# Performance work log

Hardware: AMD Instinct MI355X
Metric: run time of the kernel (lower is better)

The kernel has to match this reference:

```python
import jax, jax.numpy as jnp
import numpy as np

B, S, D, H = 2, 2048, 1024, 16
DH = D // H  # dim_per_head = 64


def setup_inputs() -> dict:
    key = jax.random.key(0)
    ks = jax.random.split(key, 12)
    scale = 1.0 / np.sqrt(D)
    inp = {
        "key": jax.random.normal(ks[0], (B, S, D), jnp.float32),
        "value": jax.random.normal(ks[1], (B, S, D), jnp.float32),
        "query": jax.random.normal(ks[2], (B, S, D), jnp.float32),
        "mask": jnp.zeros((B, S, S), dtype=bool),
        # nn.Linear weights stored as [out, in]; we keep [in, out] for x @ W
        "Wk": jax.random.normal(ks[3], (D, D), jnp.float32) * scale,
        "bk": jnp.zeros((D,), jnp.float32),
        "Wv": jax.random.normal(ks[4], (D, D), jnp.float32) * scale,
        "bv": jnp.zeros((D,), jnp.float32),
        "Wq": jax.random.normal(ks[5], (D, D), jnp.float32) * scale,
        "bq": jnp.zeros((D,), jnp.float32),
        "Wo": jax.random.normal(ks[6], (D, D), jnp.float32) * scale,
        "bo": jnp.zeros((D,), jnp.float32),
    }
    return inp


def reference(key, value, query, mask, Wk, bk, Wv, bv, Wq, bq, Wo, bo):
    # project and split heads: [B, S, D] -> [B, H, S, DH]
    def shape(x):
        return x.reshape(B, S, H, DH).transpose(0, 2, 1, 3)

    k = shape(key @ Wk + bk)
    v = shape(value @ Wv + bv)
    q = shape(query @ Wq + bq) / jnp.sqrt(jnp.asarray(DH, key.dtype))

    # scores: [B, H, Sq, Sk]
    scores = jnp.einsum("bhqd,bhkd->bhqk", q, k)
    scores = jnp.where(mask[:, None, :, :], jnp.asarray(-1e10, scores.dtype), scores)
    attn = jax.nn.softmax(scores, axis=-1)
    # dropout is identity in eval mode
    context = jnp.einsum("bhqk,bhkd->bhqd", attn, v)
    context = context.transpose(0, 2, 1, 3).reshape(B, S, D)
    output = context @ Wo + bo
    return output, attn
```

## Files before the change

kernel.cpp:

```cpp
#include <hip/hip_runtime.h>

#define B_  2
#define S_  2048
#define D_  1024
#define H_  16

typedef _Float16 h8 __attribute__((ext_vector_type(8)));
typedef _Float16 h4 __attribute__((ext_vector_type(4)));
typedef float f4 __attribute__((ext_vector_type(4)));

static __device__ __forceinline__ f4 mfma16(h8 a, h8 b, f4 c) {
  return __builtin_amdgcn_mfma_f32_16x16x32_f16(a, b, c, 0, 0, 0);
}

static __device__ __forceinline__ void gload16(const void* g, void* l) {
  __builtin_amdgcn_global_load_lds(
      (const __attribute__((address_space(1))) void*)g,
      (__attribute__((address_space(3))) void*)l, 16, 0, 0);
}

struct C3 { const float* in[3]; _Float16* out[3]; };
__global__ __launch_bounds__(256) void cvt3_kernel(C3 c) {
  const float* in = c.in[blockIdx.y];
  _Float16* out = c.out[blockIdx.y];
  const size_t i = ((size_t)blockIdx.x * 256 + threadIdx.x) * 8;
  float4 a = *(const float4*)(in + i);
  float4 b = *(const float4*)(in + i + 4);
  h8 v;
  v[0]=(_Float16)a.x; v[1]=(_Float16)a.y; v[2]=(_Float16)a.z; v[3]=(_Float16)a.w;
  v[4]=(_Float16)b.x; v[5]=(_Float16)b.y; v[6]=(_Float16)b.z; v[7]=(_Float16)b.w;
  *(h8*)(out + i) = v;
}

struct W4 { const float* w[4]; _Float16* wt[4]; };
__global__ __launch_bounds__(256) void wtrans4_kernel(W4 a) {
  const float* W = a.w[blockIdx.z];
  _Float16* WT = a.wt[blockIdx.z];
  __shared__ float tile[64][65];
  const int t = threadIdx.x;
  const int bi = blockIdx.x * 64;
  const int bj = blockIdx.y * 64;
  const int row = t >> 2, c0 = (t & 3) * 16;
  const float* src = W + (size_t)(bi + row) * D_ + bj + c0;
#pragma unroll
  for (int j = 0; j < 4; j++) {
    float4 v = *(const float4*)(src + j * 4);
    tile[row][c0 + j*4 + 0] = v.x; tile[row][c0 + j*4 + 1] = v.y;
    tile[row][c0 + j*4 + 2] = v.z; tile[row][c0 + j*4 + 3] = v.w;
  }
  __syncthreads();
  h8 o0, o1;
#pragma unroll
  for (int j = 0; j < 8; j++) o0[j] = (_Float16)tile[c0 + j][row];
#pragma unroll
  for (int j = 0; j < 8; j++) o1[j] = (_Float16)tile[c0 + 8 + j][row];
  _Float16* dst = WT + (size_t)(bj + row) * D_ + bi + c0;
  *(h8*)(dst)     = o0;
  *(h8*)(dst + 8) = o1;
}

__global__ __launch_bounds__(256) void maskflag_kernel(const unsigned char* __restrict__ mask,
                                                       unsigned char* __restrict__ flags) {
  __shared__ int s;
  const int t = threadIdx.x;
  const int kt = blockIdx.x, qb = blockIdx.y, b = blockIdx.z;
  if (t == 0) s = 0;
  __syncthreads();
  const unsigned char* mp = mask + ((size_t)(b * S_ + qb * 128 + (t >> 1))) * S_
                          + kt * 64 + (t & 1) * 32;
  const uint4* p = (const uint4*)mp;
  uint4 v = p[0], w = p[1];
  unsigned int o = v.x | v.y | v.z | v.w | w.x | w.y | w.z | w.w;
  if (o) s = 1;
  __syncthreads();
  if (t == 0) flags[((size_t)b * 16 + qb) * 32 + kt] = (unsigned char)s;
}

struct GArg { const _Float16* A; const _Float16* BT; const float* bias;
              void* out; float scale; int mode; };
struct G3 { GArg a[3]; };

__global__ __launch_bounds__(256, 3) void gemmp_kernel(G3 G) {
  const GArg g = G.a[blockIdx.z];
  const _Float16* __restrict__ A  = g.A;
  const _Float16* __restrict__ BT = g.BT;
  __shared__ _Float16 Ash[128 * 64];
  __shared__ _Float16 Bsh[128 * 64];
  const int t = threadIdx.x, lane = t & 63, wave = t >> 6;
  const int lrow = lane & 15, lq = lane >> 4;
  const int m0 = blockIdx.x * 128, n0 = blockIdx.y * 128;
  const int wm = wave >> 1, wn = wave & 1;
  f4 acc[4][4];
#pragma unroll
  for (int i = 0; i < 4; i++)
#pragma unroll
    for (int j = 0; j < 4; j++) acc[i][j] = f4{0.f, 0.f, 0.f, 0.f};
  float bb[4];
#pragma unroll
  for (int j = 0; j < 4; j++) bb[j] = g.bias[n0 + wn*64 + j*16 + lrow];

  const int srow = t >> 3;
  const int lch  = (t & 7) ^ (srow & 7);
  const _Float16* asrc = A  + (size_t)(m0 + srow) * D_ + lch * 8;
  const _Float16* bsrc = BT + (size_t)(n0 + srow) * D_ + lch * 8;

  for (int k0 = 0; k0 < D_; k0 += 64) {
#pragma unroll
    for (int rnd = 0; rnd < 4; rnd++)
      gload16(asrc + (size_t)(rnd * 32) * D_ + k0,
              (char*)Ash + rnd * 4096 + wave * 1024);
#pragma unroll
    for (int rnd = 0; rnd < 4; rnd++)
      gload16(bsrc + (size_t)(rnd * 32) * D_ + k0,
              (char*)Bsh + rnd * 4096 + wave * 1024);
    __syncthreads();
#pragma unroll
    for (int kf = 0; kf < 2; kf++) {
      h8 af[4], bf[4];
#pragma unroll
      for (int i = 0; i < 4; i++) {
        int rr = wm*64 + i*16 + lrow;
        int ch = (kf*4 + lq) ^ (rr & 7);
        af[i] = *(h8*)((char*)Ash + rr*128 + ch*16);
      }
#pragma unroll
      for (int j = 0; j < 4; j++) {
        int rr = wn*64 + j*16 + lrow;
        int ch = (kf*4 + lq) ^ (rr & 7);
        bf[j] = *(h8*)((char*)Bsh + rr*128 + ch*16);
      }
#pragma unroll
      for (int i = 0; i < 4; i++)
#pragma unroll
        for (int j = 0; j < 4; j++)
          acc[i][j] = mfma16(af[i], bf[j], acc[i][j]);
    }
    __syncthreads();
  }

  if (g.mode == 0) {
    _Float16* out = (_Float16*)g.out;
#pragma unroll
    for (int i = 0; i < 4; i++) {
      int m = m0 + wm*64 + i*16 + lq*4;
#pragma unroll
      for (int j = 0; j < 4; j++) {
        int n = n0 + wn*64 + j*16 + lrow;
#pragma unroll
        for (int r = 0; r < 4; r++)
          out[(size_t)(m + r) * D_ + n] = (_Float16)((acc[i][j][r] + bb[j]) * g.scale);
      }
    }
  } else if (g.mode == 1) {
    _Float16* out = (_Float16*)g.out;
#pragma unroll
    for (int i = 0; i < 4; i++) {
      int m = m0 + wm*64 + i*16 + lq*4;
      int b = m >> 11, s = m & (S_ - 1);
#pragma unroll
      for (int j = 0; j < 4; j++) {
        int n = n0 + wn*64 + j*16 + lrow;
        int hh = n >> 6, dh = n & 63;
        h4 hv;
#pragma unroll
        for (int r = 0; r < 4; r++) hv[r] = (_Float16)(acc[i][j][r] + bb[j]);
        *(h4*)(out + ((size_t)((b * H_ + hh) * 64 + dh)) * S_ + s) = hv;
      }
    }
  } else {
    float* out = (float*)g.out;
#pragma unroll
    for (int i = 0; i < 4; i++) {
      int m = m0 + wm*64 + i*16 + lq*4;
#pragma unroll
      for (int j = 0; j < 4; j++) {
        int n = n0 + wn*64 + j*16 + lrow;
#pragma unroll
        for (int r = 0; r < 4; r++)
          out[(size_t)(m + r) * D_ + n] = acc[i][j][r] + bb[j];
      }
    }
  }
}

__global__ __launch_bounds__(512, 4) void gemmz_kernel(G3 G) {
  const GArg g = G.a[blockIdx.z];
  const _Float16* __restrict__ A  = g.A;
  const _Float16* __restrict__ BT = g.BT;
  __shared__ _Float16 Ash[128 * 64];
  __shared__ _Float16 Bsh[128 * 64];
  const int t = threadIdx.x, lane = t & 63, wave = t >> 6;
  const int lrow = lane & 15, lq = lane >> 4;
  const int m0 = blockIdx.x * 128, n0 = blockIdx.y * 128;
  const int wm = wave >> 2, wn = wave & 3;
  f4 acc[4][2];
#pragma unroll
  for (int i = 0; i < 4; i++)
#pragma unroll
    for (int j = 0; j < 2; j++) acc[i][j] = f4{0.f, 0.f, 0.f, 0.f};
  float bb[2];
#pragma unroll
  for (int j = 0; j < 2; j++) bb[j] = g.bias[n0 + wn*32 + j*16 + lrow];

  const int srow = t >> 3;
  const int lch  = (t & 7) ^ (srow & 7);
  const _Float16* a0 = A  + (size_t)(m0 + srow)      * D_ + lch * 8;
  const _Float16* a1 = A  + (size_t)(m0 + 64 + srow) * D_ + lch * 8;
  const _Float16* b0 = BT + (size_t)(n0 + srow)      * D_ + lch * 8;
  const _Float16* b1 = BT + (size_t)(n0 + 64 + srow) * D_ + lch * 8;
  char* adst0 = (char*)Ash + wave * 1024;
  char* adst1 = (char*)Ash + 8192 + wave * 1024;
  char* bdst0 = (char*)Bsh + wave * 1024;
  char* bdst1 = (char*)Bsh + 8192 + wave * 1024;

  for (int k0 = 0; k0 < D_; k0 += 64) {
    gload16(a0 + k0, adst0);
    gload16(a1 + k0, adst1);
    gload16(b0 + k0, bdst0);
    gload16(b1 + k0, bdst1);
    __syncthreads();
#pragma unroll
    for (int kf = 0; kf < 2; kf++) {
      h8 af[4], bf[2];
#pragma unroll
      for (int i = 0; i < 4; i++) {
        int rr = wm*64 + i*16 + lrow;
        int ch = (kf*4 + lq) ^ (rr & 7);
        af[i] = *(h8*)((char*)Ash + rr*128 + ch*16);
      }
#pragma unroll
      for (int j = 0; j < 2; j++) {
        int rr = wn*32 + j*16 + lrow;
        int ch = (kf*4 + lq) ^ (rr & 7);
        bf[j] = *(h8*)((char*)Bsh + rr*128 + ch*16);
      }
#pragma unroll
      for (int i = 0; i < 4; i++)
#pragma unroll
        for (int j = 0; j < 2; j++)
          acc[i][j] = mfma16(af[i], bf[j], acc[i][j]);
    }
    __syncthreads();
  }

  if (g.mode == 0) {
    _Float16* out = (_Float16*)g.out;
#pragma unroll
    for (int i = 0; i < 4; i++) {
      int m = m0 + wm*64 + i*16 + lq*4;
#pragma unroll
      for (int j = 0; j < 2; j++) {
        int n = n0 + wn*32 + j*16 + lrow;
#pragma unroll
        for (int r = 0; r < 4; r++)
          out[(size_t)(m + r) * D_ + n] = (_Float16)((acc[i][j][r] + bb[j]) * g.scale);
      }
    }
  } else if (g.mode == 1) {
    _Float16* out = (_Float16*)g.out;
#pragma unroll
    for (int i = 0; i < 4; i++) {
      int m = m0 + wm*64 + i*16 + lq*4;
      int b = m >> 11, s = m & (S_ - 1);
#pragma unroll
      for (int j = 0; j < 2; j++) {
        int n = n0 + wn*32 + j*16 + lrow;
        int hh = n >> 6, dh = n & 63;
        h4 hv;
#pragma unroll
        for (int r = 0; r < 4; r++) hv[r] = (_Float16)(acc[i][j][r] + bb[j]);
        *(h4*)(out + ((size_t)((b * H_ + hh) * 64 + dh)) * S_ + s) = hv;
      }
    }
  } else {
    float* out = (float*)g.out;
#pragma unroll
    for (int i = 0; i < 4; i++) {
      int m = m0 + wm*64 + i*16 + lq*4;
#pragma unroll
      for (int j = 0; j < 2; j++) {
        int n = n0 + wn*32 + j*16 + lrow;
#pragma unroll
        for (int r = 0; r < 4; r++)
          out[(size_t)(m + r) * D_ + n] = acc[i][j][r] + bb[j];
      }
    }
  }
}


__global__ __launch_bounds__(256, 4) void attnA_kernel(
    const _Float16* __restrict__ Qp, const _Float16* __restrict__ Kp,
    const unsigned char* __restrict__ mask, const unsigned char* __restrict__ flags,
    float* __restrict__ Lbuf)
{
  __shared__ _Float16 Kt[256 * 64];
  const int t = threadIdx.x, lane = t & 63, wave = t >> 6;
  const int lrow = lane & 15, lq = lane >> 4;
  const int logical = ((blockIdx.x & 7) << 7) + (blockIdx.x >> 3);
  const int bh = logical >> 5, qb = logical & 31;
  const int b = bh >> 4, h = bh & 15;
  const int q0 = qb * 64, qw = q0 + wave * 16;

  h8 qf0, qf1;
  {
    const _Float16* qp = Qp + ((size_t)(b * S_ + qw + lrow)) * D_ + h * 64 + lq * 8;
    qf0 = *(const h8*)qp;
    qf1 = *(const h8*)(qp + 32);
  }

  const int srow = t >> 3, klch = (t & 7) ^ (srow & 7);
  const _Float16* ksrc = Kp + ((size_t)(b * S_ + srow)) * D_ + h * 64 + klch * 8;
  char* kdst = (char*)Kt + wave * 1024;
  const unsigned char* mflags = flags + ((size_t)(b * 16 + (qb >> 1))) * 32;

  float lsum[4] = {0.f, 0.f, 0.f, 0.f};
  for (int kt = 0; kt < S_; kt += 256) {
#pragma unroll
    for (int rnd = 0; rnd < 8; rnd++)
      gload16(ksrc + (size_t)(kt + rnd * 32) * D_, kdst + rnd * 4096);
    __syncthreads();
    const unsigned char* mrow = mask + ((size_t)(b * S_ + qw + lq*4)) * S_ + kt + lrow;
#pragma unroll
    for (int c = 0; c < 16; c++) {
      int kr = c*16 + lrow, sx = kr & 7;
      h8 k0 = *(h8*)((char*)Kt + kr*128 + ((lq     ^ sx) << 4));
      h8 k1 = *(h8*)((char*)Kt + kr*128 + (((4+lq) ^ sx) << 4));
      f4 a = f4{0.f, 0.f, 0.f, 0.f};
      a = mfma16(qf0, k0, a);
      a = mfma16(qf1, k1, a);
      if (mflags[(kt >> 6) + (c >> 2)]) {
#pragma unroll
        for (int r = 0; r < 4; r++)
          if (mrow[(size_t)r * S_ + c*16]) a[r] = -1e10f;
      }
#pragma unroll
      for (int r = 0; r < 4; r++) lsum[r] += __expf(fminf(a[r], 75.f));
    }
    __syncthreads();
  }

#pragma unroll
  for (int r = 0; r < 4; r++) {
    float cs = lsum[r];
#pragma unroll
    for (int d = 1; d < 16; d <<= 1) cs += __shfl_xor(cs, d);
    if (lrow == 0) Lbuf[((size_t)bh << 11) + qw + lq*4 + r] = 1.0f / cs;
  }
}

__global__ __launch_bounds__(256, 4) void attnB_kernel(
    const _Float16* __restrict__ Qp, const _Float16* __restrict__ Kp,
    const _Float16* __restrict__ VpT, const unsigned char* __restrict__ mask,
    const unsigned char* __restrict__ flags, const float* __restrict__ Lbuf,
    float* __restrict__ attn, _Float16* __restrict__ CtxH)
{
  __shared__ _Float16 Kt[128 * 64];
  __shared__ _Float16 Vt[64 * 128];
  __shared__ _Float16 Pt[64 * 64];
  const int t = threadIdx.x, lane = t & 63, wave = t >> 6;
  const int lrow = lane & 15, lq = lane >> 4;
  const int logical = ((blockIdx.x & 7) << 7) + (blockIdx.x >> 3);
  const int bh = logical >> 5, qb = logical & 31;
  const int b = bh >> 4, h = bh & 15;
  const int q0 = qb * 64, qw = q0 + wave * 16;

  h8 qf0, qf1;
  {
    const _Float16* qp = Qp + ((size_t)(b * S_ + qw + lrow)) * D_ + h * 64 + lq * 8;
    qf0 = *(const h8*)qp;
    qf1 = *(const h8*)(qp + 32);
  }
  float li[4];
#pragma unroll
  for (int r = 0; r < 4; r++) li[r] = Lbuf[((size_t)bh << 11) + qw + lq*4 + r];

  const int srow = t >> 3, klch = (t & 7) ^ (srow & 7);
  const _Float16* ksrc = Kp + ((size_t)(b * S_ + srow)) * D_ + h * 64 + klch * 8;
  char* kdst = (char*)Kt + wave * 1024;
  const int vrow = t >> 4, vlch = (t & 15) ^ (vrow & 15);
  const _Float16* vsrc = VpT + (size_t)bh * 64 * S_ + (size_t)vrow * S_ + vlch * 8;
  char* vdst = (char*)Vt + wave * 1024;
  const unsigned char* mflags = flags + ((size_t)(b * 16 + (qb >> 1))) * 32;

  f4 ctx[4];
#pragma unroll
  for (int dt = 0; dt < 4; dt++) ctx[dt] = f4{0.f, 0.f, 0.f, 0.f};

  for (int kt = 0; kt < S_; kt += 128) {
#pragma unroll
    for (int rnd = 0; rnd < 4; rnd++)
      gload16(ksrc + (size_t)(kt + rnd * 32) * D_, kdst + rnd * 4096);
#pragma unroll
    for (int rnd = 0; rnd < 4; rnd++)
      gload16(vsrc + (size_t)(rnd * 16) * S_ + kt, vdst + rnd * 4096);
    __syncthreads();

#pragma unroll
    for (int hh = 0; hh < 2; hh++) {
      const int kbase = kt + hh * 64;
      const bool mf = mflags[kbase >> 6] != 0;
      const unsigned char* mrow = mask + ((size_t)(b * S_ + qw + lq*4)) * S_ + kbase + lrow;
      const int prw = wave*16 + lq*4;
#pragma unroll
      for (int c = 0; c < 4; c++) {
        int kr = hh*64 + c*16 + lrow, sx = kr & 7;
        h8 k0 = *(h8*)((char*)Kt + kr*128 + ((lq     ^ sx) << 4));
        h8 k1 = *(h8*)((char*)Kt + kr*128 + (((4+lq) ^ sx) << 4));
        f4 a = f4{0.f, 0.f, 0.f, 0.f};
        a = mfma16(qf0, k0, a);
        a = mfma16(qf1, k1, a);
        if (mf) {
#pragma unroll
          for (int r = 0; r < 4; r++)
            if (mrow[(size_t)r * S_ + c*16]) a[r] = -1e10f;
        }
        float* ap = attn + ((size_t)bh * S_ + qw + lq*4) * S_ + kbase + c*16 + lrow;
        int eb = c*32 + lrow*2;
#pragma unroll
        for (int r = 0; r < 4; r++) {
          float p = __expf(fminf(a[r], 75.f)) * li[r];
          ap[(size_t)r * S_] = p;
          int rw = prw + r;
          *(_Float16*)((char*)Pt + rw*128 + ((((eb >> 4) ^ (rw & 7))) << 4) + (eb & 15))
              = (_Float16)p;
        }
      }
      {
        int pr2 = wave*16 + lrow, sxp = pr2 & 7;
        h8 pf0 = *(h8*)((char*)Pt + pr2*128 + (((    lq) ^ sxp) << 4));
        h8 pf1 = *(h8*)((char*)Pt + pr2*128 + (((4 + lq) ^ sxp) << 4));
#pragma unroll
        for (int dt = 0; dt < 4; dt++) {
          int vr = dt*16 + lrow, sxv = vr & 15;
          h8 vf0 = *(h8*)((char*)Vt + vr*256 + (((hh*8     + lq) ^ sxv) << 4));
          h8 vf1 = *(h8*)((char*)Vt + vr*256 + (((hh*8 + 4 + lq) ^ sxv) << 4));
          ctx[dt] = mfma16(pf0, vf0, ctx[dt]);
          ctx[dt] = mfma16(pf1, vf1, ctx[dt]);
        }
      }
    }
    __syncthreads();
  }

  _Float16* cp = CtxH + ((size_t)(b * S_ + qw + lq*4)) * D_ + h * 64 + lrow;
#pragma unroll
  for (int dt = 0; dt < 4; dt++)
#pragma unroll
    for (int r = 0; r < 4; r++)
      cp[(size_t)r * D_ + dt*16] = (_Float16)ctx[dt][r];
}

extern "C" void kernel_launch(void* const* d_in, const int* in_sizes, int n_in,
                              void* d_out, int out_size, void* d_ws, size_t ws_size,
                              hipStream_t stream) {
  const float* key   = (const float*)d_in[0];
  const float* value = (const float*)d_in[1];
  const float* query = (const float*)d_in[2];
  const unsigned char* mask = (const unsigned char*)d_in[3];
  const float* Wk = (const float*)d_in[4];
  const float* bk = (const float*)d_in[5];
  const float* Wv = (const float*)d_in[6];
  const float* bv = (const float*)d_in[7];
  const float* Wq = (const float*)d_in[8];
  const float* bq = (const float*)d_in[9];
  const float* Wo = (const float*)d_in[10];
  const float* bo = (const float*)d_in[11];

  char* ws = (char*)d_ws;
  _Float16* WkT  = (_Float16*)(ws + 0);
  _Float16* WvT  = (_Float16*)(ws + (size_t)2  * 1024 * 1024);
  _Float16* WqT  = (_Float16*)(ws + (size_t)4  * 1024 * 1024);
  _Float16* WoT  = (_Float16*)(ws + (size_t)6  * 1024 * 1024);
  _Float16* Qp   = (_Float16*)(ws + (size_t)8  * 1024 * 1024);
  _Float16* Kp   = (_Float16*)(ws + (size_t)16 * 1024 * 1024);
  _Float16* VpT  = (_Float16*)(ws + (size_t)24 * 1024 * 1024);
  _Float16* CtxH = (_Float16*)(ws + (size_t)32 * 1024 * 1024);
  unsigned char* flags = (unsigned char*)(ws + (size_t)40 * 1024 * 1024);
  float* Lbuf = (float*)(ws + (size_t)40 * 1024 * 1024 + 64 * 1024);

  float* outp = (float*)d_out;
  float* attn = outp + (size_t)B_ * S_ * D_;
  _Float16* qH = (_Float16*)(attn);
  _Float16* kH = (_Float16*)((char*)attn + (size_t)8  * 1024 * 1024);
  _Float16* vH = (_Float16*)((char*)attn + (size_t)16 * 1024 * 1024);

  C3 c{{query, key, value}, {qH, kH, vH}};
  cvt3_kernel<<<dim3(2048, 3), 256, 0, stream>>>(c);

  W4 w{{Wk, Wv, Wq, Wo}, {WkT, WvT, WqT, WoT}};
  wtrans4_kernel<<<dim3(16, 16, 4), 256, 0, stream>>>(w);

  maskflag_kernel<<<dim3(32, 16, 2), 256, 0, stream>>>(mask, flags);

  G3 gp{{{qH, WqT, bq, Qp, 0.125f, 0},
         {kH, WkT, bk, Kp, 1.0f,   0},
         {vH, WvT, bv, VpT, 1.0f,  1}}};
  gemmp_kernel<<<dim3(32, 8, 3), 256, 0, stream>>>(gp);

  attnA_kernel<<<1024, 256, 0, stream>>>(Qp, Kp, mask, flags, Lbuf);
  attnB_kernel<<<1024, 256, 0, stream>>>(Qp, Kp, VpT, mask, flags, Lbuf, attn, CtxH);

  G3 go{{{CtxH, WoT, bo, outp, 1.0f, 2},
         {nullptr, nullptr, nullptr, nullptr, 0.f, 2},
         {nullptr, nullptr, nullptr, nullptr, 0.f, 2}}};
  gemmz_kernel<<<dim3(32, 8, 1), 512, 0, stream>>>(go);
}
```

Measured before the change: 298.0 us.

## Fuse attention row-sum and output passes into one kernel with MFMA priority

Merges the two attention kernels into one. Each block first computes the softmax denominators over all keys, then reuses them in registers for the second pass that writes the attention probabilities and context, with one shared-memory buffer holding both phases. This drops a kernel launch and the round trip of the normalizer buffer through global memory, and reloads Q only once. It also raises wave priority around the MFMA sections so matrix work is issued ahead of other waves. Shared memory grows to 40KB per block, which may limit how many blocks fit on each CU.

```diff
diff --git a/kernel.cpp b/kernel.cpp
--- a/kernel.cpp
+++ b/kernel.cpp
@@ -288,13 +288,13 @@
   }
 }
 
-
-__global__ __launch_bounds__(256, 4) void attnA_kernel(
+__global__ __launch_bounds__(256, 4) void attnF_kernel(
     const _Float16* __restrict__ Qp, const _Float16* __restrict__ Kp,
-    const unsigned char* __restrict__ mask, const unsigned char* __restrict__ flags,
-    float* __restrict__ Lbuf)
+    const _Float16* __restrict__ VpT, const unsigned char* __restrict__ mask,
+    const unsigned char* __restrict__ flags,
+    float* __restrict__ attn, _Float16* __restrict__ CtxH)
 {
-  __shared__ _Float16 Kt[256 * 64];
+  __shared__ char smem[40960];
   const int t = threadIdx.x, lane = t & 63, wave = t >> 6;
   const int lrow = lane & 15, lq = lane >> 4;
   const int logical = ((blockIdx.x & 7) << 7) + (blockIdx.x >> 3);
@@ -311,8 +311,9 @@
 
   const int srow = t >> 3, klch = (t & 7) ^ (srow & 7);
   const _Float16* ksrc = Kp + ((size_t)(b * S_ + srow)) * D_ + h * 64 + klch * 8;
-  char* kdst = (char*)Kt + wave * 1024;
+  char* kdst = smem + wave * 1024;
   const unsigned char* mflags = flags + ((size_t)(b * 16 + (qb >> 1))) * 32;
+  const unsigned char* mrow0 = mask + ((size_t)(b * S_ + qw + lq*4)) * S_ + lrow;
 
   float lsum[4] = {0.f, 0.f, 0.f, 0.f};
   for (int kt = 0; kt < S_; kt += 256) {
@@ -320,19 +321,20 @@
     for (int rnd = 0; rnd < 8; rnd++)
       gload16(ksrc + (size_t)(kt + rnd * 32) * D_, kdst + rnd * 4096);
     __syncthreads();
-    const unsigned char* mrow = mask + ((size_t)(b * S_ + qw + lq*4)) * S_ + kt + lrow;
 #pragma unroll
     for (int c = 0; c < 16; c++) {
       int kr = c*16 + lrow, sx = kr & 7;
-      h8 k0 = *(h8*)((char*)Kt + kr*128 + ((lq     ^ sx) << 4));
-      h8 k1 = *(h8*)((char*)Kt + kr*128 + (((4+lq) ^ sx) << 4));
+      h8 k0 = *(h8*)(smem + kr*128 + ((lq     ^ sx) << 4));
+      h8 k1 = *(h8*)(smem + kr*128 + (((4+lq) ^ sx) << 4));
       f4 a = f4{0.f, 0.f, 0.f, 0.f};
+      __builtin_amdgcn_s_setprio(1);
       a = mfma16(qf0, k0, a);
       a = mfma16(qf1, k1, a);
+      __builtin_amdgcn_s_setprio(0);
       if (mflags[(kt >> 6) + (c >> 2)]) {
 #pragma unroll
         for (int r = 0; r < 4; r++)
-          if (mrow[(size_t)r * S_ + c*16]) a[r] = -1e10f;
+          if (mrow0[(size_t)r * S_ + kt + c*16]) a[r] = -1e10f;
       }
 #pragma unroll
       for (int r = 0; r < 4; r++) lsum[r] += __expf(fminf(a[r], 75.f));
@@ -340,48 +342,20 @@
     __syncthreads();
   }
 
+  float li[4];
 #pragma unroll
   for (int r = 0; r < 4; r++) {
     float cs = lsum[r];
 #pragma unroll
     for (int d = 1; d < 16; d <<= 1) cs += __shfl_xor(cs, d);
-    if (lrow == 0) Lbuf[((size_t)bh << 11) + qw + lq*4 + r] = 1.0f / cs;
-  }
-}
-
-__global__ __launch_bounds__(256, 4) void attnB_kernel(
-    const _Float16* __restrict__ Qp, const _Float16* __restrict__ Kp,
-    const _Float16* __restrict__ VpT, const unsigned char* __restrict__ mask,
-    const unsigned char* __restrict__ flags, const float* __restrict__ Lbuf,
-    float* __restrict__ attn, _Float16* __restrict__ CtxH)
-{
-  __shared__ _Float16 Kt[128 * 64];
-  __shared__ _Float16 Vt[64 * 128];
-  __shared__ _Float16 Pt[64 * 64];
-  const int t = threadIdx.x, lane = t & 63, wave = t >> 6;
-  const int lrow = lane & 15, lq = lane >> 4;
-  const int logical = ((blockIdx.x & 7) << 7) + (blockIdx.x >> 3);
-  const int bh = logical >> 5, qb = logical & 31;
-  const int b = bh >> 4, h = bh & 15;
-  const int q0 = qb * 64, qw = q0 + wave * 16;
-
-  h8 qf0, qf1;
-  {
-    const _Float16* qp = Qp + ((size_t)(b * S_ + qw + lrow)) * D_ + h * 64 + lq * 8;
-    qf0 = *(const h8*)qp;
-    qf1 = *(const h8*)(qp + 32);
-  }
-  float li[4];
-#pragma unroll
-  for (int r = 0; r < 4; r++) li[r] = Lbuf[((size_t)bh << 11) + qw + lq*4 + r];
-
-  const int srow = t >> 3, klch = (t & 7) ^ (srow & 7);
-  const _Float16* ksrc = Kp + ((size_t)(b * S_ + srow)) * D_ + h * 64 + klch * 8;
-  char* kdst = (char*)Kt + wave * 1024;
+    li[r] = 1.0f / cs;
+  }
+
+  char* const Vt = smem + 16384;
+  char* const Pt = smem + 32768;
   const int vrow = t >> 4, vlch = (t & 15) ^ (vrow & 15);
   const _Float16* vsrc = VpT + (size_t)bh * 64 * S_ + (size_t)vrow * S_ + vlch * 8;
-  char* vdst = (char*)Vt + wave * 1024;
-  const unsigned char* mflags = flags + ((size_t)(b * 16 + (qb >> 1))) * 32;
+  char* vdst = Vt + wave * 1024;
 
   f4 ctx[4];
 #pragma unroll
@@ -400,20 +374,21 @@
     for (int hh = 0; hh < 2; hh++) {
       const int kbase = kt + hh * 64;
       const bool mf = mflags[kbase >> 6] != 0;
-      const unsigned char* mrow = mask + ((size_t)(b * S_ + qw + lq*4)) * S_ + kbase + lrow;
       const int prw = wave*16 + lq*4;
 #pragma unroll
       for (int c = 0; c < 4; c++) {
         int kr = hh*64 + c*16 + lrow, sx = kr & 7;
-        h8 k0 = *(h8*)((char*)Kt + kr*128 + ((lq     ^ sx) << 4));
-        h8 k1 = *(h8*)((char*)Kt + kr*128 + (((4+lq) ^ sx) << 4));
+        h8 k0 = *(h8*)(smem + kr*128 + ((lq     ^ sx) << 4));
+        h8 k1 = *(h8*)(smem + kr*128 + (((4+lq) ^ sx) << 4));
         f4 a = f4{0.f, 0.f, 0.f, 0.f};
+        __builtin_amdgcn_s_setprio(1);
         a = mfma16(qf0, k0, a);
         a = mfma16(qf1, k1, a);
+        __builtin_amdgcn_s_setprio(0);
         if (mf) {
 #pragma unroll
           for (int r = 0; r < 4; r++)
-            if (mrow[(size_t)r * S_ + c*16]) a[r] = -1e10f;
+            if (mrow0[(size_t)r * S_ + kbase + c*16]) a[r] = -1e10f;
         }
         float* ap = attn + ((size_t)bh * S_ + qw + lq*4) * S_ + kbase + c*16 + lrow;
         int eb = c*32 + lrow*2;
@@ -422,22 +397,24 @@
           float p = __expf(fminf(a[r], 75.f)) * li[r];
           ap[(size_t)r * S_] = p;
           int rw = prw + r;
-          *(_Float16*)((char*)Pt + rw*128 + ((((eb >> 4) ^ (rw & 7))) << 4) + (eb & 15))
+          *(_Float16*)(Pt + rw*128 + ((((eb >> 4) ^ (rw & 7))) << 4) + (eb & 15))
               = (_Float16)p;
         }
       }
       {
         int pr2 = wave*16 + lrow, sxp = pr2 & 7;
-        h8 pf0 = *(h8*)((char*)Pt + pr2*128 + (((    lq) ^ sxp) << 4));
-        h8 pf1 = *(h8*)((char*)Pt + pr2*128 + (((4 + lq) ^ sxp) << 4));
+        h8 pf0 = *(h8*)(Pt + pr2*128 + (((    lq) ^ sxp) << 4));
+        h8 pf1 = *(h8*)(Pt + pr2*128 + (((4 + lq) ^ sxp) << 4));
+        __builtin_amdgcn_s_setprio(1);
 #pragma unroll
         for (int dt = 0; dt < 4; dt++) {
           int vr = dt*16 + lrow, sxv = vr & 15;
-          h8 vf0 = *(h8*)((char*)Vt + vr*256 + (((hh*8     + lq) ^ sxv) << 4));
-          h8 vf1 = *(h8*)((char*)Vt + vr*256 + (((hh*8 + 4 + lq) ^ sxv) << 4));
+          h8 vf0 = *(h8*)(Vt + vr*256 + (((hh*8     + lq) ^ sxv) << 4));
+          h8 vf1 = *(h8*)(Vt + vr*256 + (((hh*8 + 4 + lq) ^ sxv) << 4));
           ctx[dt] = mfma16(pf0, vf0, ctx[dt]);
           ctx[dt] = mfma16(pf1, vf1, ctx[dt]);
         }
+        __builtin_amdgcn_s_setprio(0);
       }
     }
     __syncthreads();
@@ -477,7 +454,6 @@
   _Float16* VpT  = (_Float16*)(ws + (size_t)24 * 1024 * 1024);
   _Float16* CtxH = (_Float16*)(ws + (size_t)32 * 1024 * 1024);
   unsigned char* flags = (unsigned char*)(ws + (size_t)40 * 1024 * 1024);
-  float* Lbuf = (float*)(ws + (size_t)40 * 1024 * 1024 + 64 * 1024);
 
   float* outp = (float*)d_out;
   float* attn = outp + (size_t)B_ * S_ * D_;
@@ -498,8 +474,7 @@
          {vH, WvT, bv, VpT, 1.0f,  1}}};
   gemmp_kernel<<<dim3(32, 8, 3), 256, 0, stream>>>(gp);
 
-  attnA_kernel<<<1024, 256, 0, stream>>>(Qp, Kp, mask, flags, Lbuf);
-  attnB_kernel<<<1024, 256, 0, stream>>>(Qp, Kp, VpT, mask, flags, Lbuf, attn, CtxH);
+  attnF_kernel<<<1024, 256, 0, stream>>>(Qp, Kp, VpT, mask, flags, attn, CtxH);
 
   G3 go{{{CtxH, WoT, bo, outp, 1.0f, 2},
          {nullptr, nullptr, nullptr, nullptr, 0.f, 2},
```

Result: faster. 279.0 us (-6.4%).
